# Performance work log

Measured on AMD Instinct MI355X. Metric: run time of the kernel, lower is better.

## Reference

```python
import jax, jax.numpy as jnp
import numpy as np

B, T, E, H, V = 64, 32, 512, 512, 16000


def setup_inputs() -> dict:
    key = jax.random.key(0)
    ks = jax.random.split(key, 9)
    s_e = 1.0 / np.sqrt(E)
    s_h = 1.0 / np.sqrt(H)
    return {
        "features": jax.random.normal(ks[0], (B, E), dtype=jnp.float32),
        "captions": jax.random.randint(ks[1], (B, T), 0, V, dtype=jnp.int64),
        "emb": jax.random.normal(ks[2], (V, E), dtype=jnp.float32) * 0.02,
        "W_ih": jax.random.normal(ks[3], (4 * H, E), dtype=jnp.float32) * s_e,
        "W_hh": jax.random.normal(ks[4], (4 * H, H), dtype=jnp.float32) * s_h,
        "b_ih": jax.random.normal(ks[5], (4 * H,), dtype=jnp.float32) * s_h,
        "b_hh": jax.random.normal(ks[6], (4 * H,), dtype=jnp.float32) * s_h,
        "W_lin": jax.random.normal(ks[7], (V, H), dtype=jnp.float32) * s_h,
        "b_lin": jax.random.normal(ks[8], (V,), dtype=jnp.float32) * s_h,
    }


def reference(features, captions, emb, W_ih, W_hh, b_ih, b_hh, W_lin, b_lin):
    # features: [B, E]; captions: [B, T] int. Faithful to original: input at
    # t=0 is features, at t>=1 it is embedding(captions[:, t]) (not t-1).
    Bn, Tn = captions.shape
    Hn = W_hh.shape[1]
    emb_cap = emb[captions]                                   # [B, T, E]
    x_seq = jnp.concatenate([features[:, None, :], emb_cap[:, 1:, :]], axis=1)
    # Precompute input projection for all timesteps: [B, T, 4H]
    x_proj = jnp.einsum("bte,ge->btg", x_seq, W_ih) + b_ih + b_hh

    def step(carry, xp_t):                                    # xp_t: [B, 4H]
        h, c = carry
        gates = xp_t + h @ W_hh.T
        i, f, g, o = jnp.split(gates, 4, axis=-1)             # PyTorch ifgo order
        i = jax.nn.sigmoid(i)
        f = jax.nn.sigmoid(f)
        g = jnp.tanh(g)
        o = jax.nn.sigmoid(o)
        c = f * c + i * g
        h = o * jnp.tanh(c)
        return (h, c), h

    h0 = jnp.zeros((Bn, Hn), dtype=features.dtype)
    c0 = jnp.zeros((Bn, Hn), dtype=features.dtype)
    _, hs = jax.lax.scan(step, (h0, c0), jnp.swapaxes(x_proj, 0, 1))  # hs: [T, B, H]
    hs = jnp.swapaxes(hs, 0, 1)                               # [B, T, H]
    logits = jnp.einsum("bth,vh->btv", hs, W_lin) + b_lin     # [B, T, V]
    return logits
```

## Files before the change

### kernel.cpp

```cpp
#include <hip/hip_runtime.h>
#include <hip/hip_bf16.h>


typedef __attribute__((ext_vector_type(8))) short short8v;
typedef __attribute__((ext_vector_type(4))) short short4v;
typedef __attribute__((ext_vector_type(4))) float float4v;
typedef __attribute__((ext_vector_type(4))) int   int4v;

static __device__ __forceinline__ short f2bf(float v) {
    __hip_bfloat16 b = __float2bfloat16(v);
    return *reinterpret_cast<short*>(&b);
}
static __device__ __forceinline__ float bf2f(short s) {
    __hip_bfloat16 b = *reinterpret_cast<__hip_bfloat16*>(&s);
    return __bfloat162float(b);
}


__global__ __launch_bounds__(256) void prep_x_kernel(
    const float* __restrict__ features, const int* __restrict__ captions,
    const float* __restrict__ emb, short* __restrict__ A1)
{
    int m = blockIdx.x;
    int t = m >> 6, b = m & 63;
    const float* src = (t == 0) ? (features + (long)b * 512)
                                : (emb + (long)captions[b * 32 + t] * 512);
    long base = (long)m * 1536;
    for (int k = threadIdx.x; k < 512; k += 256) {
        float v = src[k];
        short hi = f2bf(v);
        short lo = f2bf(v - bf2f(hi));
        A1[base + k]        = hi;
        A1[base + 512 + k]  = lo;
        A1[base + 1024 + k] = hi;
    }
}

__global__ __launch_bounds__(256) void prep_w_kernel(
    const float* __restrict__ W_ih, short* __restrict__ B1)
{
    int n = blockIdx.x;
    long base = (long)n * 1536;
    const float* src = W_ih + (long)n * 512;
    for (int k = threadIdx.x; k < 512; k += 256) {
        float v = src[k];
        short hi = f2bf(v);
        short lo = f2bf(v - bf2f(hi));
        B1[base + k]        = hi;
        B1[base + 512 + k]  = hi;
        B1[base + 1024 + k] = lo;
    }
}

__global__ __launch_bounds__(256) void prep_bias_kernel(
    const float* __restrict__ b_ih, const float* __restrict__ b_hh,
    float* __restrict__ biasc, int* __restrict__ flags)
{
    int g = blockIdx.x * 256 + threadIdx.x;
    if (g < 2048) biasc[g] = b_ih[g] + b_hh[g];
    if (g < 640)  flags[g] = 0;
}

__global__ __launch_bounds__(256) void prep_wlin_kernel(
    const float* __restrict__ W_lin, short* __restrict__ Wl)
{
    int v = blockIdx.x;
    long base = (long)v * 512;
    for (int k = threadIdx.x; k < 512; k += 256) {
        Wl[base + k] = f2bf(W_lin[base + k]);
    }
}

#define AF2_FRAGS 8192
#define W3_FRAGS_PER_BLK 4096

static __device__ __forceinline__ int frag2_idx(int tile, int k, int row15, int isLo)
{
    return ((tile * 32 + (k >> 5) + isLo * 16) * 64
            + ((k >> 2) & 3) * 16 + row15) * 8
           + (k & 3) + ((k >> 4) & 1) * 4;
}

#define GBK 64
#define GPAD 8
#define GLDT (GBK + GPAD)

__global__ __launch_bounds__(512, 1) void fused_lstm_logits_kernel(
    float* __restrict__ x_proj, const float* __restrict__ W_hh,
    const short* __restrict__ A1, const short* __restrict__ B1,
    const float* __restrict__ biasc,
    short* __restrict__ Af, short* __restrict__ hs2,
    int* __restrict__ flags, const short* __restrict__ Wl,
    const float* __restrict__ b_lin, float* __restrict__ out)
{
    __shared__ __align__(16) short Wf[W3_FRAGS_PER_BLK * 8];
    __shared__ float gl[32 * 65];
    __shared__ short Hs[64][12];
    __shared__ short Ls[64][12];
    __shared__ short As[128 * GLDT];
    __shared__ short Bs[128 * GLDT];

    const int tid  = threadIdx.x;
    const int bid  = blockIdx.x;
    const int lane = tid & 63;
    const int wave = tid >> 6;
    const int r    = lane & 15, q = lane >> 4;
    const int frep   = (bid & 7) * 64;
    const int frep16 = (bid & 7) * 16;
    int* __restrict__ xpc = flags + 512;

    if (bid < 64) {
        const int mt   = wave & 3;
        const int nt   = wave >> 2;
        const int j0   = bid * 8;
        const int aq   = bid & 3;
        const int kt0  = bid >> 2;

        for (int i = 0; i < 32; ++i) {
            int nl = i;
            int s2 = nl >> 3, u2 = nl & 7;
            int nt2 = nl >> 4, rr2 = nl & 15;
            float v = W_hh[((long)s2 * 512 + j0 + u2) * 512 + tid];
            short hi2 = f2bf(v);
            short lo2 = f2bf(v - bf2f(hi2));
            Wf[frag2_idx(nt2, tid, rr2, 0)] = hi2;
            Wf[frag2_idx(nt2, tid, rr2, 1)] = lo2;
        }
        __syncthreads();

        const int bb  = lane;
        const int ub  = wave;
        const int jj  = j0 + ub;
        float c_reg = 0.0f;

        const int rdt  = (tid >> 7) & 1;
        const int rmt  = (tid >> 5) & 3;
        const int rrb  = (tid >> 1) & 15;
        const int rhf  = tid & 1;
        const int rbb  = rmt * 16 + rrb;
        const int rq5  = (2 * aq + rhf) & 3;
        const size_t rfrag =
            (size_t)((rmt * 32 + kt0 + rdt * 16) * 64 + rq5 * 16 + rrb);
        const size_t roff = rfrag * 8 + (size_t)(aq >> 1) * 4;

        const short8v* Bw = (const short8v*)Wf + nt * 32 * 64 + lane;

        if (tid == 0) {
            while (__hip_atomic_load(&xpc[frep16 + 0], __ATOMIC_RELAXED,
                                     __HIP_MEMORY_SCOPE_AGENT) < 16)
                __builtin_amdgcn_s_sleep(4);
        }
        __syncthreads();

        float xc0, xc1, xc2, xc3;
        {
            const float* xp = x_proj + ((size_t)0 * 64 + bb) * 2048 + jj;
            xc0 = xp[0]; xc1 = xp[512]; xc2 = xp[1024]; xc3 = xp[1536];
        }
        int xpn = 16;

        for (int t = 0; t < 32; ++t) {
            float xn0 = 0.f, xn1 = 0.f, xn2 = 0.f, xn3 = 0.f;
            if (t < 31) {
                int nbm = (t + 1) >> 1;
                if (xpn < 16) {
                    while (__hip_atomic_load(&xpc[frep16 + nbm], __ATOMIC_RELAXED,
                                             __HIP_MEMORY_SCOPE_AGENT) < 16)
                        __builtin_amdgcn_s_sleep(2);
                }
                const float* xp = x_proj + ((size_t)(t + 1) * 64 + bb) * 2048 + jj;
                xn0 = xp[0]; xn1 = xp[512]; xn2 = xp[1024]; xn3 = xp[1536];
                int fbm = (t + 2) >> 1; if (fbm > 15) fbm = 15;
                xpn = __hip_atomic_load(&xpc[frep16 + fbm], __ATOMIC_RELAXED,
                                        __HIP_MEMORY_SCOPE_AGENT);
            }

            float4v acc = (float4v)(0.0f);
            if (t > 0) {
                const short8v* Ab = (const short8v*)Af
                    + (size_t)(t - 1) * AF2_FRAGS + mt * 32 * 64 + lane;
                short8v Ahi[16], Alo[16];

                unsigned long long ready;
                {
                    int myf = __hip_atomic_load(&flags[frep + lane], __ATOMIC_RELAXED,
                                                __HIP_MEMORY_SCOPE_AGENT);
                    ready = __ballot(myf >= t);
                }
#pragma unroll
                for (int g = 0; g < 4; ++g) {
                    const unsigned long long need = 0xFFFFull << (g * 16);
                    while ((ready & need) != need) {
                        int myf = __hip_atomic_load(&flags[frep + lane], __ATOMIC_RELAXED,
                                                    __HIP_MEMORY_SCOPE_AGENT);
                        ready = __ballot(myf >= t);
                    }
                    asm volatile("" ::: "memory");
#pragma unroll
                    for (int k = 0; k < 4; ++k) {
                        Ahi[g * 4 + k] = Ab[(g * 4 + k) * 64];
                        Alo[g * 4 + k] = Ab[(16 + g * 4 + k) * 64];
                    }
                }

                float4v a0 = (float4v)(0.0f), a1 = (float4v)(0.0f), a2 = (float4v)(0.0f);
#pragma unroll
                for (int kt = 0; kt < 16; ++kt) {
                    short8v Bhi = Bw[kt * 64];
                    short8v Blo = Bw[(16 + kt) * 64];
                    a0 = __builtin_amdgcn_mfma_f32_16x16x32_bf16(Ahi[kt], Bhi, a0, 0, 0, 0);
                    a1 = __builtin_amdgcn_mfma_f32_16x16x32_bf16(Alo[kt], Bhi, a1, 0, 0, 0);
                    a2 = __builtin_amdgcn_mfma_f32_16x16x32_bf16(Ahi[kt], Blo, a2, 0, 0, 0);
                }
                acc = a0 + a1 + a2;
            }

            __syncthreads();
#pragma unroll
            for (int reg = 0; reg < 4; ++reg)
                gl[(nt * 16 + r) * 65 + mt * 16 + q * 4 + reg] = acc[reg];
            __syncthreads();

            float iv = gl[(0  + ub) * 65 + bb] + xc0;
            float fv = gl[(8  + ub) * 65 + bb] + xc1;
            float gv = gl[(16 + ub) * 65 + bb] + xc2;
            float ov = gl[(24 + ub) * 65 + bb] + xc3;
            float ig = 1.f / (1.f + __expf(-iv));
            float fg = 1.f / (1.f + __expf(-fv));
            float gg = tanhf(gv);
            float og = 1.f / (1.f + __expf(-ov));
            float cn = fg * c_reg + ig * gg;
            float hn = og * tanhf(cn);
            c_reg = cn;

            short hi = f2bf(hn);
            Hs[bb][ub] = hi;
            if (t < 31) Ls[bb][ub] = f2bf(hn - bf2f(hi));
            __syncthreads();

            if (tid < 256) {
                if (t < 31) {
                    const short* src = rdt ? &Ls[rbb][rhf * 4] : &Hs[rbb][rhf * 4];
                    short s0 = src[0], s1 = src[1], s2 = src[2], s3 = src[3];
                    unsigned lo32 = (unsigned short)s0 | ((unsigned)(unsigned short)s1 << 16);
                    unsigned hi32 = (unsigned short)s2 | ((unsigned)(unsigned short)s3 << 16);
                    long long pv = ((long long)hi32 << 32) | (long long)lo32;
                    short* dst = Af + (size_t)t * (AF2_FRAGS * 8) + roff;
                    asm volatile("global_store_dwordx2 %0, %1, off sc0 sc1"
                                 :: "v"(dst), "v"(pv) : "memory");
                }
                if (tid < 64) {
                    const short* hp = &Hs[tid][0];
                    int4v pv;
                    pv.x = (int)((unsigned short)hp[0] | ((unsigned)(unsigned short)hp[1] << 16));
                    pv.y = (int)((unsigned short)hp[2] | ((unsigned)(unsigned short)hp[3] << 16));
                    pv.z = (int)((unsigned short)hp[4] | ((unsigned)(unsigned short)hp[5] << 16));
                    pv.w = (int)((unsigned short)hp[6] | ((unsigned)(unsigned short)hp[7] << 16));
                    char* dst2 = (char*)(hs2 + ((size_t)t * 64 + tid) * 512 + j0);
                    asm volatile("global_store_dwordx4 %0, %1, off sc0 sc1"
                                 :: "v"(dst2), "v"(pv) : "memory");
                }
                asm volatile("s_waitcnt vmcnt(0)" ::: "memory");
            }
            __syncthreads();
            if (tid == 0) {
#pragma unroll
                for (int rp = 0; rp < 8; ++rp)
                    __hip_atomic_store(&flags[rp * 64 + bid], t + 1,
                                       __ATOMIC_RELAXED, __HIP_MEMORY_SCOPE_AGENT);
            }

            xc0 = xn0; xc1 = xn1; xc2 = xn2; xc3 = xn3;
        }
    } else {
        const int w   = bid - 64;
        const int wm2 = wave >> 2;
        const int wn2 = wave & 3;

        for (int task = w; task < 2256; task += 192) {
            if (task < 256) {
                const int bm = task >> 4;
                const int bn = task & 15;

                float4v acc[4][2];
#pragma unroll
                for (int i = 0; i < 4; ++i)
#pragma unroll
                    for (int j = 0; j < 2; ++j) acc[i][j] = (float4v)(0.0f);

                const long arow0 = (long)bm * 128;
                const long brow0 = (long)bn * 128;

                for (int kt = 0; kt < 1536; kt += GBK) {
                    __syncthreads();
#pragma unroll
                    for (int it = 0; it < 2; ++it) {
                        int t2 = tid + it * 512;
                        int row = t2 >> 3, seg = t2 & 7;
                        const short* gA = A1 + (arow0 + row) * 1536L + kt + seg * 8;
                        *(short8v*)&As[row * GLDT + seg * 8] = *(const short8v*)gA;
                        const short* gB = B1 + (brow0 + row) * 1536L + kt + seg * 8;
                        *(short8v*)&Bs[row * GLDT + seg * 8] = *(const short8v*)gB;
                    }
                    __syncthreads();
#pragma unroll
                    for (int kc = 0; kc < GBK; kc += 32) {
                        short8v af[4], bf[2];
#pragma unroll
                        for (int i = 0; i < 4; ++i) {
                            int arow = wm2 * 64 + i * 16 + r;
                            union { short4v h[2]; short8v v; } ua;
                            ua.h[0] = *(short4v*)&As[arow * GLDT + kc + q * 4];
                            ua.h[1] = *(short4v*)&As[arow * GLDT + kc + 16 + q * 4];
                            af[i] = ua.v;
                        }
#pragma unroll
                        for (int j = 0; j < 2; ++j) {
                            int brow = wn2 * 32 + j * 16 + r;
                            union { short4v h[2]; short8v v; } ub;
                            ub.h[0] = *(short4v*)&Bs[brow * GLDT + kc + q * 4];
                            ub.h[1] = *(short4v*)&Bs[brow * GLDT + kc + 16 + q * 4];
                            bf[j] = ub.v;
                        }
#pragma unroll
                        for (int i = 0; i < 4; ++i)
#pragma unroll
                            for (int j = 0; j < 2; ++j)
                                acc[i][j] = __builtin_amdgcn_mfma_f32_16x16x32_bf16(
                                    af[i], bf[j], acc[i][j], 0, 0, 0);
                    }
                }

#pragma unroll
                for (int j = 0; j < 2; ++j) {
                    int col = bn * 128 + wn2 * 32 + j * 16 + r;
                    float bv = biasc[col];
#pragma unroll
                    for (int i = 0; i < 4; ++i) {
                        int row0 = bm * 128 + wm2 * 64 + i * 16 + q * 4;
#pragma unroll
                        for (int reg = 0; reg < 4; ++reg) {
                            float vv = acc[i][j][reg] + bv;
                            float* dst = x_proj + (size_t)(row0 + reg) * 2048 + col;
                            asm volatile("global_store_dword %0, %1, off sc0 sc1"
                                         :: "v"(dst), "v"(vv) : "memory");
                        }
                    }
                }
                asm volatile("s_waitcnt vmcnt(0)" ::: "memory");
                __syncthreads();
                if (tid == 0) {
#pragma unroll
                    for (int rp = 0; rp < 8; ++rp)
                        __hip_atomic_fetch_add(&xpc[rp * 16 + bm], 1,
                                               __ATOMIC_RELAXED,
                                               __HIP_MEMORY_SCOPE_AGENT);
                }
            } else {
                const int lt = task - 256;
                const int bm = lt / 125;
                const int bn = lt % 125;
                const int target = 2 * bm + 2;

                if (tid < 64) {
                    while (true) {
                        int f = __hip_atomic_load(&flags[frep + tid], __ATOMIC_RELAXED,
                                                  __HIP_MEMORY_SCOPE_AGENT);
                        if (!__any(f < target)) break;
                        __builtin_amdgcn_s_sleep(16);
                    }
                }
                __syncthreads();

                float4v acc[4][2];
#pragma unroll
                for (int i = 0; i < 4; ++i)
#pragma unroll
                    for (int j = 0; j < 2; ++j) acc[i][j] = (float4v)(0.0f);

                const long arow0 = (long)bm * 128;
                const long brow0 = (long)bn * 128;

                for (int kt = 0; kt < 512; kt += GBK) {
                    __syncthreads();
#pragma unroll
                    for (int it = 0; it < 2; ++it) {
                        int t2 = tid + it * 512;
                        int row = t2 >> 3, seg = t2 & 7;
                        const short* gA = hs2 + (arow0 + row) * 512L + kt + seg * 8;
                        *(short8v*)&As[row * GLDT + seg * 8] = *(const short8v*)gA;
                        const short* gB = Wl + (brow0 + row) * 512L + kt + seg * 8;
                        *(short8v*)&Bs[row * GLDT + seg * 8] = *(const short8v*)gB;
                    }
                    __syncthreads();
#pragma unroll
                    for (int kc = 0; kc < GBK; kc += 32) {
                        short8v af[4], bf[2];
#pragma unroll
                        for (int i = 0; i < 4; ++i) {
                            int arow = wm2 * 64 + i * 16 + r;
                            union { short4v h[2]; short8v v; } ua;
                            ua.h[0] = *(short4v*)&As[arow * GLDT + kc + q * 4];
                            ua.h[1] = *(short4v*)&As[arow * GLDT + kc + 16 + q * 4];
                            af[i] = ua.v;
                        }
#pragma unroll
                        for (int j = 0; j < 2; ++j) {
                            int brow = wn2 * 32 + j * 16 + r;
                            union { short4v h[2]; short8v v; } ub;
                            ub.h[0] = *(short4v*)&Bs[brow * GLDT + kc + q * 4];
                            ub.h[1] = *(short4v*)&Bs[brow * GLDT + kc + 16 + q * 4];
                            bf[j] = ub.v;
                        }
#pragma unroll
                        for (int i = 0; i < 4; ++i)
#pragma unroll
                            for (int j = 0; j < 2; ++j)
                                acc[i][j] = __builtin_amdgcn_mfma_f32_16x16x32_bf16(
                                    af[i], bf[j], acc[i][j], 0, 0, 0);
                    }
                }

#pragma unroll
                for (int j = 0; j < 2; ++j) {
                    int col = bn * 128 + wn2 * 32 + j * 16 + r;
                    float bv = b_lin[col];
#pragma unroll
                    for (int i = 0; i < 4; ++i) {
                        int lr0 = wm2 * 64 + i * 16 + q * 4;
#pragma unroll
                        for (int reg = 0; reg < 4; ++reg) {
                            int m  = bm * 128 + lr0 + reg;
                            int tt = m >> 6, bb2 = m & 63;
                            out[((long)bb2 * 32 + tt) * 16000 + col] = acc[i][j][reg] + bv;
                        }
                    }
                }
            }
            __syncthreads();
        }
    }
}

extern "C" void kernel_launch(void* const* d_in, const int* in_sizes, int n_in,
                              void* d_out, int out_size, void* d_ws, size_t ws_size,
                              hipStream_t stream) {
    const float* features = (const float*)d_in[0];
    const int*   captions = (const int*)d_in[1];
    const float* emb      = (const float*)d_in[2];
    const float* W_ih     = (const float*)d_in[3];
    const float* W_hh     = (const float*)d_in[4];
    const float* b_ih     = (const float*)d_in[5];
    const float* b_hh     = (const float*)d_in[6];
    const float* W_lin    = (const float*)d_in[7];
    const float* b_lin    = (const float*)d_in[8];
    float* out = (float*)d_out;

    char* ws = (char*)d_ws;
    float* x_proj = (float*)ws;  ws += 2048L * 2048 * 4;
    short* A1     = (short*)ws;  ws += 2048L * 1536 * 2;
    short* B1     = (short*)ws;  ws += 2048L * 1536 * 2;
    short* Wl     = (short*)ws;  ws += 16000L * 512 * 2;
    short* hs2    = (short*)ws;  ws += 2048L * 512 * 2;
    float* biasc  = (float*)ws;  ws += 2048 * 4;
    int*   flags  = (int*)ws;    ws += 4096;
    short* Af2    = (short*)ws;  ws += 31L * AF2_FRAGS * 8 * 2;

    prep_x_kernel<<<2048, 256, 0, stream>>>(features, captions, emb, A1);
    prep_w_kernel<<<2048, 256, 0, stream>>>(W_ih, B1);
    prep_bias_kernel<<<8, 256, 0, stream>>>(b_ih, b_hh, biasc, flags);
    prep_wlin_kernel<<<16000, 256, 0, stream>>>(W_lin, Wl);

    fused_lstm_logits_kernel<<<256, 512, 0, stream>>>(
        x_proj, W_hh, A1, B1, biasc, Af2, hs2, flags, Wl, b_lin, out);
}
```

Baseline: 248.6 us.

## Split-K input projection with atomics and reuse fragment h-buffer for logits GEMM

The input-projection GEMM tasks are split into two K halves (512 tasks instead of 256) that accumulate into a zero-initialised x_proj via atomicAdd, with the bias moved into the LSTM gate read. Readiness counters now wait for 32 contributions instead of 16. The separate hs2 buffer is dropped: the logits GEMM reads A operands straight from the MFMA-fragment-layout hi buffer Af, now allocated for all 32 timesteps, so the LDS staging of A and one global store per step go away. The trade-offs are atomic traffic on x_proj, an extra zeroing pass in prep, and float reordering from the split-K sums.

```diff
diff --git a/kernel.cpp b/kernel.cpp
--- a/kernel.cpp
+++ b/kernel.cpp
@@ -19,7 +19,8 @@
 
 __global__ __launch_bounds__(256) void prep_x_kernel(
     const float* __restrict__ features, const int* __restrict__ captions,
-    const float* __restrict__ emb, short* __restrict__ A1)
+    const float* __restrict__ emb, short* __restrict__ A1,
+    float* __restrict__ x_proj)
 {
     int m = blockIdx.x;
     int t = m >> 6, b = m & 63;
@@ -34,6 +35,9 @@
         A1[base + 512 + k]  = lo;
         A1[base + 1024 + k] = hi;
     }
+    float4v z = {0.f, 0.f, 0.f, 0.f};
+    for (int k = threadIdx.x; k < 512; k += 256)
+        *(float4v*)&x_proj[(long)m * 2048 + k * 4] = z;
 }
 
 __global__ __launch_bounds__(256) void prep_w_kernel(
@@ -89,9 +93,9 @@
     float* __restrict__ x_proj, const float* __restrict__ W_hh,
     const short* __restrict__ A1, const short* __restrict__ B1,
     const float* __restrict__ biasc,
-    short* __restrict__ Af, short* __restrict__ hs2,
-    int* __restrict__ flags, const short* __restrict__ Wl,
-    const float* __restrict__ b_lin, float* __restrict__ out)
+    short* __restrict__ Af, int* __restrict__ flags,
+    const short* __restrict__ Wl, const float* __restrict__ b_lin,
+    float* __restrict__ out)
 {
     __shared__ __align__(16) short Wf[W3_FRAGS_PER_BLK * 8];
     __shared__ float gl[32 * 65];
@@ -133,6 +137,11 @@
         const int jj  = j0 + ub;
         float c_reg = 0.0f;
 
+        const float bc0 = biasc[jj];
+        const float bc1 = biasc[512 + jj];
+        const float bc2 = biasc[1024 + jj];
+        const float bc3 = biasc[1536 + jj];
+
         const int rdt  = (tid >> 7) & 1;
         const int rmt  = (tid >> 5) & 3;
         const int rrb  = (tid >> 1) & 15;
@@ -147,7 +156,7 @@
 
         if (tid == 0) {
             while (__hip_atomic_load(&xpc[frep16 + 0], __ATOMIC_RELAXED,
-                                     __HIP_MEMORY_SCOPE_AGENT) < 16)
+                                     __HIP_MEMORY_SCOPE_AGENT) < 32)
                 __builtin_amdgcn_s_sleep(4);
         }
         __syncthreads();
@@ -155,21 +164,23 @@
         float xc0, xc1, xc2, xc3;
         {
             const float* xp = x_proj + ((size_t)0 * 64 + bb) * 2048 + jj;
-            xc0 = xp[0]; xc1 = xp[512]; xc2 = xp[1024]; xc3 = xp[1536];
+            xc0 = xp[0] + bc0; xc1 = xp[512] + bc1;
+            xc2 = xp[1024] + bc2; xc3 = xp[1536] + bc3;
         }
-        int xpn = 16;
+        int xpn = 32;
 
         for (int t = 0; t < 32; ++t) {
             float xn0 = 0.f, xn1 = 0.f, xn2 = 0.f, xn3 = 0.f;
             if (t < 31) {
                 int nbm = (t + 1) >> 1;
-                if (xpn < 16) {
+                if (xpn < 32) {
                     while (__hip_atomic_load(&xpc[frep16 + nbm], __ATOMIC_RELAXED,
-                                             __HIP_MEMORY_SCOPE_AGENT) < 16)
+                                             __HIP_MEMORY_SCOPE_AGENT) < 32)
                         __builtin_amdgcn_s_sleep(2);
                 }
                 const float* xp = x_proj + ((size_t)(t + 1) * 64 + bb) * 2048 + jj;
-                xn0 = xp[0]; xn1 = xp[512]; xn2 = xp[1024]; xn3 = xp[1536];
+                xn0 = xp[0] + bc0; xn1 = xp[512] + bc1;
+                xn2 = xp[1024] + bc2; xn3 = xp[1536] + bc3;
                 int fbm = (t + 2) >> 1; if (fbm > 15) fbm = 15;
                 xpn = __hip_atomic_load(&xpc[frep16 + fbm], __ATOMIC_RELAXED,
                                         __HIP_MEMORY_SCOPE_AGENT);
@@ -235,31 +246,18 @@
 
             short hi = f2bf(hn);
             Hs[bb][ub] = hi;
-            if (t < 31) Ls[bb][ub] = f2bf(hn - bf2f(hi));
+            Ls[bb][ub] = f2bf(hn - bf2f(hi));
             __syncthreads();
 
             if (tid < 256) {
-                if (t < 31) {
-                    const short* src = rdt ? &Ls[rbb][rhf * 4] : &Hs[rbb][rhf * 4];
-                    short s0 = src[0], s1 = src[1], s2 = src[2], s3 = src[3];
-                    unsigned lo32 = (unsigned short)s0 | ((unsigned)(unsigned short)s1 << 16);
-                    unsigned hi32 = (unsigned short)s2 | ((unsigned)(unsigned short)s3 << 16);
-                    long long pv = ((long long)hi32 << 32) | (long long)lo32;
-                    short* dst = Af + (size_t)t * (AF2_FRAGS * 8) + roff;
-                    asm volatile("global_store_dwordx2 %0, %1, off sc0 sc1"
-                                 :: "v"(dst), "v"(pv) : "memory");
-                }
-                if (tid < 64) {
-                    const short* hp = &Hs[tid][0];
-                    int4v pv;
-                    pv.x = (int)((unsigned short)hp[0] | ((unsigned)(unsigned short)hp[1] << 16));
-                    pv.y = (int)((unsigned short)hp[2] | ((unsigned)(unsigned short)hp[3] << 16));
-                    pv.z = (int)((unsigned short)hp[4] | ((unsigned)(unsigned short)hp[5] << 16));
-                    pv.w = (int)((unsigned short)hp[6] | ((unsigned)(unsigned short)hp[7] << 16));
-                    char* dst2 = (char*)(hs2 + ((size_t)t * 64 + tid) * 512 + j0);
-                    asm volatile("global_store_dwordx4 %0, %1, off sc0 sc1"
-                                 :: "v"(dst2), "v"(pv) : "memory");
-                }
+                const short* src = rdt ? &Ls[rbb][rhf * 4] : &Hs[rbb][rhf * 4];
+                short s0 = src[0], s1 = src[1], s2 = src[2], s3 = src[3];
+                unsigned lo32 = (unsigned short)s0 | ((unsigned)(unsigned short)s1 << 16);
+                unsigned hi32 = (unsigned short)s2 | ((unsigned)(unsigned short)s3 << 16);
+                long long pv = ((long long)hi32 << 32) | (long long)lo32;
+                short* dst = Af + (size_t)t * (AF2_FRAGS * 8) + roff;
+                asm volatile("global_store_dwordx2 %0, %1, off sc0 sc1"
+                             :: "v"(dst), "v"(pv) : "memory");
                 asm volatile("s_waitcnt vmcnt(0)" ::: "memory");
             }
             __syncthreads();
@@ -277,10 +275,12 @@
         const int wm2 = wave >> 2;
         const int wn2 = wave & 3;
 
-        for (int task = w; task < 2256; task += 192) {
-            if (task < 256) {
-                const int bm = task >> 4;
-                const int bn = task & 15;
+        for (int task = w; task < 2512; task += 192) {
+            if (task < 512) {
+                const int bm   = task >> 5;
+                const int sub  = task & 31;
+                const int bn   = sub >> 1;
+                const int kseg = sub & 1;
 
                 float4v acc[4][2];
 #pragma unroll
@@ -290,16 +290,17 @@
 
                 const long arow0 = (long)bm * 128;
                 const long brow0 = (long)bn * 128;
-
-                for (int kt = 0; kt < 1536; kt += GBK) {
+                const long kbase = (long)kseg * 768;
+
+                for (int kt = 0; kt < 768; kt += GBK) {
                     __syncthreads();
 #pragma unroll
                     for (int it = 0; it < 2; ++it) {
                         int t2 = tid + it * 512;
                         int row = t2 >> 3, seg = t2 & 7;
-                        const short* gA = A1 + (arow0 + row) * 1536L + kt + seg * 8;
+                        const short* gA = A1 + (arow0 + row) * 1536L + kbase + kt + seg * 8;
                         *(short8v*)&As[row * GLDT + seg * 8] = *(const short8v*)gA;
-                        const short* gB = B1 + (brow0 + row) * 1536L + kt + seg * 8;
+                        const short* gB = B1 + (brow0 + row) * 1536L + kbase + kt + seg * 8;
                         *(short8v*)&Bs[row * GLDT + seg * 8] = *(const short8v*)gB;
                     }
                     __syncthreads();
@@ -334,16 +335,13 @@
 #pragma unroll
                 for (int j = 0; j < 2; ++j) {
                     int col = bn * 128 + wn2 * 32 + j * 16 + r;
-                    float bv = biasc[col];
 #pragma unroll
                     for (int i = 0; i < 4; ++i) {
                         int row0 = bm * 128 + wm2 * 64 + i * 16 + q * 4;
 #pragma unroll
                         for (int reg = 0; reg < 4; ++reg) {
-                            float vv = acc[i][j][reg] + bv;
-                            float* dst = x_proj + (size_t)(row0 + reg) * 2048 + col;
-                            asm volatile("global_store_dword %0, %1, off sc0 sc1"
-                                         :: "v"(dst), "v"(vv) : "memory");
+                            atomicAdd(&x_proj[(size_t)(row0 + reg) * 2048 + col],
+                                      acc[i][j][reg]);
                         }
                     }
                 }
@@ -357,7 +355,7 @@
                                                __HIP_MEMORY_SCOPE_AGENT);
                 }
             } else {
-                const int lt = task - 256;
+                const int lt = task - 512;
                 const int bm = lt / 125;
                 const int bn = lt % 125;
                 const int target = 2 * bm + 2;
@@ -378,8 +376,9 @@
 #pragma unroll
                     for (int j = 0; j < 2; ++j) acc[i][j] = (float4v)(0.0f);
 
-                const long arow0 = (long)bm * 128;
                 const long brow0 = (long)bn * 128;
+                const short8v* Abase = (const short8v*)Af
+                    + (size_t)(2 * bm + wm2) * AF2_FRAGS + lane;
 
                 for (int kt = 0; kt < 512; kt += GBK) {
                     __syncthreads();
@@ -387,23 +386,17 @@
                     for (int it = 0; it < 2; ++it) {
                         int t2 = tid + it * 512;
                         int row = t2 >> 3, seg = t2 & 7;
-                        const short* gA = hs2 + (arow0 + row) * 512L + kt + seg * 8;
-                        *(short8v*)&As[row * GLDT + seg * 8] = *(const short8v*)gA;
                         const short* gB = Wl + (brow0 + row) * 512L + kt + seg * 8;
                         *(short8v*)&Bs[row * GLDT + seg * 8] = *(const short8v*)gB;
                     }
                     __syncthreads();
 #pragma unroll
                     for (int kc = 0; kc < GBK; kc += 32) {
+                        const int ktile = (kt + kc) >> 5;
                         short8v af[4], bf[2];
 #pragma unroll
-                        for (int i = 0; i < 4; ++i) {
-                            int arow = wm2 * 64 + i * 16 + r;
-                            union { short4v h[2]; short8v v; } ua;
-                            ua.h[0] = *(short4v*)&As[arow * GLDT + kc + q * 4];
-                            ua.h[1] = *(short4v*)&As[arow * GLDT + kc + 16 + q * 4];
-                            af[i] = ua.v;
-                        }
+                        for (int i = 0; i < 4; ++i)
+                            af[i] = Abase[(size_t)i * 32 * 64 + ktile * 64];
 #pragma unroll
                         for (int j = 0; j < 2; ++j) {
                             int brow = wn2 * 32 + j * 16 + r;
@@ -461,16 +454,15 @@
     short* A1     = (short*)ws;  ws += 2048L * 1536 * 2;
     short* B1     = (short*)ws;  ws += 2048L * 1536 * 2;
     short* Wl     = (short*)ws;  ws += 16000L * 512 * 2;
-    short* hs2    = (short*)ws;  ws += 2048L * 512 * 2;
     float* biasc  = (float*)ws;  ws += 2048 * 4;
     int*   flags  = (int*)ws;    ws += 4096;
-    short* Af2    = (short*)ws;  ws += 31L * AF2_FRAGS * 8 * 2;
-
-    prep_x_kernel<<<2048, 256, 0, stream>>>(features, captions, emb, A1);
+    short* Af2    = (short*)ws;  ws += 32L * AF2_FRAGS * 8 * 2;
+
+    prep_x_kernel<<<2048, 256, 0, stream>>>(features, captions, emb, A1, x_proj);
     prep_w_kernel<<<2048, 256, 0, stream>>>(W_ih, B1);
     prep_bias_kernel<<<8, 256, 0, stream>>>(b_ih, b_hh, biasc, flags);
     prep_wlin_kernel<<<16000, 256, 0, stream>>>(W_lin, Wl);
 
     fused_lstm_logits_kernel<<<256, 512, 0, stream>>>(
-        x_proj, W_hh, A1, B1, biasc, Af2, hs2, flags, Wl, b_lin, out);
-}
+        x_proj, W_hh, A1, B1, biasc, Af2, flags, Wl, b_lin, out);
+}
```

After: 256.0 us. +3.0%, slower.

## Split input-projection GEMM into finer tasks and decouple hs store from recurrence flags

Applied to the files above, without the earlier changes.

The x_proj GEMM task grid is split into twice as many narrower tiles (128x64 instead of 128x128), so the 192 worker blocks produce the first timesteps' input projections sooner and the recurrent blocks start earlier. The recurrence now publishes its step flag right after the Af fragment stores, and the hs2 store for the logits GEMM trails it. The logits-task readiness target shifts by one to match, and a final flag value of 33 marks completion. The cost is more tasks with lower per-task MFMA reuse and some added sync logic.

```diff
diff --git a/kernel.cpp b/kernel.cpp
--- a/kernel.cpp
+++ b/kernel.cpp
@@ -73,6 +73,7 @@
 
 #define AF2_FRAGS 8192
 #define W3_FRAGS_PER_BLK 4096
+#define XPC_TARGET 32
 
 static __device__ __forceinline__ int frag2_idx(int tile, int k, int row15, int isLo)
 {
@@ -147,7 +148,7 @@
 
         if (tid == 0) {
             while (__hip_atomic_load(&xpc[frep16 + 0], __ATOMIC_RELAXED,
-                                     __HIP_MEMORY_SCOPE_AGENT) < 16)
+                                     __HIP_MEMORY_SCOPE_AGENT) < XPC_TARGET)
                 __builtin_amdgcn_s_sleep(4);
         }
         __syncthreads();
@@ -157,15 +158,15 @@
             const float* xp = x_proj + ((size_t)0 * 64 + bb) * 2048 + jj;
             xc0 = xp[0]; xc1 = xp[512]; xc2 = xp[1024]; xc3 = xp[1536];
         }
-        int xpn = 16;
+        int xpn = XPC_TARGET;
 
         for (int t = 0; t < 32; ++t) {
             float xn0 = 0.f, xn1 = 0.f, xn2 = 0.f, xn3 = 0.f;
             if (t < 31) {
                 int nbm = (t + 1) >> 1;
-                if (xpn < 16) {
+                if (xpn < XPC_TARGET) {
                     while (__hip_atomic_load(&xpc[frep16 + nbm], __ATOMIC_RELAXED,
-                                             __HIP_MEMORY_SCOPE_AGENT) < 16)
+                                             __HIP_MEMORY_SCOPE_AGENT) < XPC_TARGET)
                         __builtin_amdgcn_s_sleep(2);
                 }
                 const float* xp = x_proj + ((size_t)(t + 1) * 64 + bb) * 2048 + jj;
@@ -238,8 +239,8 @@
             if (t < 31) Ls[bb][ub] = f2bf(hn - bf2f(hi));
             __syncthreads();
 
-            if (tid < 256) {
-                if (t < 31) {
+            if (t < 31) {
+                if (tid < 256) {
                     const short* src = rdt ? &Ls[rbb][rhf * 4] : &Hs[rbb][rhf * 4];
                     short s0 = src[0], s1 = src[1], s2 = src[2], s3 = src[3];
                     unsigned lo32 = (unsigned short)s0 | ((unsigned)(unsigned short)s1 << 16);
@@ -248,26 +249,36 @@
                     short* dst = Af + (size_t)t * (AF2_FRAGS * 8) + roff;
                     asm volatile("global_store_dwordx2 %0, %1, off sc0 sc1"
                                  :: "v"(dst), "v"(pv) : "memory");
-                }
-                if (tid < 64) {
-                    const short* hp = &Hs[tid][0];
-                    int4v pv;
-                    pv.x = (int)((unsigned short)hp[0] | ((unsigned)(unsigned short)hp[1] << 16));
-                    pv.y = (int)((unsigned short)hp[2] | ((unsigned)(unsigned short)hp[3] << 16));
-                    pv.z = (int)((unsigned short)hp[4] | ((unsigned)(unsigned short)hp[5] << 16));
-                    pv.w = (int)((unsigned short)hp[6] | ((unsigned)(unsigned short)hp[7] << 16));
-                    char* dst2 = (char*)(hs2 + ((size_t)t * 64 + tid) * 512 + j0);
-                    asm volatile("global_store_dwordx4 %0, %1, off sc0 sc1"
-                                 :: "v"(dst2), "v"(pv) : "memory");
-                }
+                    asm volatile("s_waitcnt vmcnt(0)" ::: "memory");
+                }
+                __syncthreads();
+                if (tid == 0) {
+#pragma unroll
+                    for (int rp = 0; rp < 8; ++rp)
+                        __hip_atomic_store(&flags[rp * 64 + bid], t + 1,
+                                           __ATOMIC_RELAXED, __HIP_MEMORY_SCOPE_AGENT);
+                }
+            }
+            if (tid < 64) {
+                const short* hp = &Hs[tid][0];
+                int4v pv;
+                pv.x = (int)((unsigned short)hp[0] | ((unsigned)(unsigned short)hp[1] << 16));
+                pv.y = (int)((unsigned short)hp[2] | ((unsigned)(unsigned short)hp[3] << 16));
+                pv.z = (int)((unsigned short)hp[4] | ((unsigned)(unsigned short)hp[5] << 16));
+                pv.w = (int)((unsigned short)hp[6] | ((unsigned)(unsigned short)hp[7] << 16));
+                char* dst2 = (char*)(hs2 + ((size_t)t * 64 + tid) * 512 + j0);
+                asm volatile("global_store_dwordx4 %0, %1, off sc0 sc1"
+                             :: "v"(dst2), "v"(pv) : "memory");
+            }
+            if (t == 31) {
                 asm volatile("s_waitcnt vmcnt(0)" ::: "memory");
-            }
-            __syncthreads();
-            if (tid == 0) {
-#pragma unroll
-                for (int rp = 0; rp < 8; ++rp)
-                    __hip_atomic_store(&flags[rp * 64 + bid], t + 1,
-                                       __ATOMIC_RELAXED, __HIP_MEMORY_SCOPE_AGENT);
+                __syncthreads();
+                if (tid == 0) {
+#pragma unroll
+                    for (int rp = 0; rp < 8; ++rp)
+                        __hip_atomic_store(&flags[rp * 64 + bid], 33,
+                                           __ATOMIC_RELAXED, __HIP_MEMORY_SCOPE_AGENT);
+                }
             }
 
             xc0 = xn0; xc1 = xn1; xc2 = xn2; xc3 = xn3;
@@ -277,19 +288,17 @@
         const int wm2 = wave >> 2;
         const int wn2 = wave & 3;
 
-        for (int task = w; task < 2256; task += 192) {
-            if (task < 256) {
-                const int bm = task >> 4;
-                const int bn = task & 15;
-
-                float4v acc[4][2];
-#pragma unroll
-                for (int i = 0; i < 4; ++i)
-#pragma unroll
-                    for (int j = 0; j < 2; ++j) acc[i][j] = (float4v)(0.0f);
+        for (int task = w; task < 2512; task += 192) {
+            if (task < 512) {
+                const int bm  = task >> 5;
+                const int sub = task & 31;
+                const long nbase = (long)sub * 64;
+
+                float4v acc[4];
+#pragma unroll
+                for (int i = 0; i < 4; ++i) acc[i] = (float4v)(0.0f);
 
                 const long arow0 = (long)bm * 128;
-                const long brow0 = (long)bn * 128;
 
                 for (int kt = 0; kt < 1536; kt += GBK) {
                     __syncthreads();
@@ -299,13 +308,16 @@
                         int row = t2 >> 3, seg = t2 & 7;
                         const short* gA = A1 + (arow0 + row) * 1536L + kt + seg * 8;
                         *(short8v*)&As[row * GLDT + seg * 8] = *(const short8v*)gA;
-                        const short* gB = B1 + (brow0 + row) * 1536L + kt + seg * 8;
+                    }
+                    {
+                        int row = tid >> 3, seg = tid & 7;
+                        const short* gB = B1 + (nbase + row) * 1536L + kt + seg * 8;
                         *(short8v*)&Bs[row * GLDT + seg * 8] = *(const short8v*)gB;
                     }
                     __syncthreads();
 #pragma unroll
                     for (int kc = 0; kc < GBK; kc += 32) {
-                        short8v af[4], bf[2];
+                        short8v af[4], bf;
 #pragma unroll
                         for (int i = 0; i < 4; ++i) {
                             int arow = wm2 * 64 + i * 16 + r;
@@ -314,33 +326,29 @@
                             ua.h[1] = *(short4v*)&As[arow * GLDT + kc + 16 + q * 4];
                             af[i] = ua.v;
                         }
-#pragma unroll
-                        for (int j = 0; j < 2; ++j) {
-                            int brow = wn2 * 32 + j * 16 + r;
+                        {
+                            int brow = wn2 * 16 + r;
                             union { short4v h[2]; short8v v; } ub;
                             ub.h[0] = *(short4v*)&Bs[brow * GLDT + kc + q * 4];
                             ub.h[1] = *(short4v*)&Bs[brow * GLDT + kc + 16 + q * 4];
-                            bf[j] = ub.v;
+                            bf = ub.v;
                         }
 #pragma unroll
                         for (int i = 0; i < 4; ++i)
-#pragma unroll
-                            for (int j = 0; j < 2; ++j)
-                                acc[i][j] = __builtin_amdgcn_mfma_f32_16x16x32_bf16(
-                                    af[i], bf[j], acc[i][j], 0, 0, 0);
-                    }
-                }
-
-#pragma unroll
-                for (int j = 0; j < 2; ++j) {
-                    int col = bn * 128 + wn2 * 32 + j * 16 + r;
+                            acc[i] = __builtin_amdgcn_mfma_f32_16x16x32_bf16(
+                                af[i], bf, acc[i], 0, 0, 0);
+                    }
+                }
+
+                {
+                    int col = (int)nbase + wn2 * 16 + r;
                     float bv = biasc[col];
 #pragma unroll
                     for (int i = 0; i < 4; ++i) {
                         int row0 = bm * 128 + wm2 * 64 + i * 16 + q * 4;
 #pragma unroll
                         for (int reg = 0; reg < 4; ++reg) {
-                            float vv = acc[i][j][reg] + bv;
+                            float vv = acc[i][reg] + bv;
                             float* dst = x_proj + (size_t)(row0 + reg) * 2048 + col;
                             asm volatile("global_store_dword %0, %1, off sc0 sc1"
                                          :: "v"(dst), "v"(vv) : "memory");
@@ -357,10 +365,10 @@
                                                __HIP_MEMORY_SCOPE_AGENT);
                 }
             } else {
-                const int lt = task - 256;
+                const int lt = task - 512;
                 const int bm = lt / 125;
                 const int bn = lt % 125;
-                const int target = 2 * bm + 2;
+                const int target = 2 * bm + 3;
 
                 if (tid < 64) {
                     while (true) {
```

Measured after the change: 254.4 us. +2.4%, slower.
